# Kernel optimization log

Hardware: AMD Instinct MI355X
Metric: run time of the kernel (lower is better)

## Reference

```python
import jax, jax.numpy as jnp
import numpy as np

F = 16384   # n_features
D = 768     # d_model
B = 2       # batch
S = 256     # seq len
C = 16      # connections per downstream feature
M = F * C   # total connections


def setup_inputs() -> dict:
    key = jax.random.key(0)
    k1, k2, k3, k4 = jax.random.split(key, 4)
    up_facts = jax.random.normal(k1, (B, S, F), dtype=jnp.float32)
    down_encoder = jax.random.normal(k2, (F, D), dtype=jnp.float32) * 0.02
    up_decoder = jax.random.normal(k3, (D, F), dtype=jnp.float32) * 0.02
    # connection_mask.nonzero() is row-major: i sorted, C targets per row
    i_indices = jnp.repeat(jnp.arange(F, dtype=jnp.int32), C)  # [M]
    j_indices = jax.random.randint(k4, (M,), 0, F, dtype=jnp.int32)  # [M]
    return {
        "up_facts": up_facts,
        "down_encoder": down_encoder,
        "up_decoder": up_decoder,
        "i_indices": i_indices,
        "j_indices": j_indices,
    }


def reference(up_facts, down_encoder, up_decoder, i_indices, j_indices):
    # up_facts: [B,S,F]; down_encoder: [F,D]; up_decoder: [D,F]
    b, s, f = up_facts.shape
    m = i_indices.shape[0]
    # per-connection virtual weight: values[m] = down_encoder[i[m]] . up_decoder[:, j[m]]
    values = jnp.einsum("md,dm->m", down_encoder[i_indices], up_decoder[:, j_indices])  # [M]
    # gather upstream feature activations and scale
    scaled = up_facts[:, :, j_indices] * values[None, None, :]  # [B,S,M]
    # scatter_add over last axis into downstream feature bins (i is constant across B,S)
    flat = scaled.reshape(b * s, m).T  # [M, B*S]
    contrib = jax.ops.segment_sum(flat, i_indices, num_segments=f)  # [F, B*S]
    return contrib.T.reshape(b, s, f)
```

## Files before the change

kernel.cpp:

```cpp
#include <hip/hip_runtime.h>
#include <hip/hip_bf16.h>

#define F_ 16384
#define D_ 768
#define C_ 16
#define BS_ 512
#define M_ (F_*C_)
#define NCHUNK 8
#define CDIM 96

static __device__ __forceinline__ float bf2f(unsigned short u) {
    return __uint_as_float(((unsigned int)u) << 16);
}
static __device__ __forceinline__ unsigned short f2bf(float f) {
    return __bfloat16_as_ushort(__float2bfloat16(f));
}

__global__ __launch_bounds__(256) void k_transpose_chunked(const float* __restrict__ in,
                                                           unsigned short* __restrict__ decC) {
    __shared__ float tile[64][65];
    int c4 = threadIdx.x & 15;
    int r  = threadIdx.x >> 4;
    int fbase = blockIdx.x * 64;
    int dbase = blockIdx.y * 64;
#pragma unroll
    for (int k = 0; k < 4; ++k) {
        int drow = r + k * 16;
        float4 v = *(const float4*)(in + (size_t)(dbase + drow) * F_ + fbase + c4 * 4);
        tile[drow][c4 * 4 + 0] = v.x;
        tile[drow][c4 * 4 + 1] = v.y;
        tile[drow][c4 * 4 + 2] = v.z;
        tile[drow][c4 * 4 + 3] = v.w;
    }
    __syncthreads();
    int dp = threadIdx.x & 15;
    int fr = threadIdx.x >> 4;
#pragma unroll
    for (int k = 0; k < 4; ++k) {
        int frow = fr + k * 16;
        float v0 = tile[4 * dp + 0][frow];
        float v1 = tile[4 * dp + 1][frow];
        float v2 = tile[4 * dp + 2][frow];
        float v3 = tile[4 * dp + 3][frow];
        uint2 p;
        p.x = ((unsigned int)f2bf(v1) << 16) | (unsigned int)f2bf(v0);
        p.y = ((unsigned int)f2bf(v3) << 16) | (unsigned int)f2bf(v2);
        int d  = dbase + dp * 4;
        int c  = d / CDIM;
        int dl = d - c * CDIM;
        *(uint2*)(decC + ((size_t)c * F_ + (fbase + frow)) * CDIM + dl) = p;
    }
}

__global__ __launch_bounds__(256) void k_values_chunked(const float* __restrict__ enc,
                                                        const unsigned short* __restrict__ decC,
                                                        const int* __restrict__ jidx,
                                                        float* __restrict__ partial) {
    __shared__ float encS[64 * CDIM];
    int chunk = blockIdx.x & 7;
    int mblk  = blockIdx.x >> 3;
    int m0 = mblk * 1024;
    int f0 = mblk * 64;

    {
        float4* s4 = (float4*)encS;
        const float* eb = enc + (size_t)f0 * D_ + chunk * CDIM;
#pragma unroll
        for (int k = 0; k < 6; ++k) {
            int idx = threadIdx.x + k * 256;
            int row = idx / 24;
            int col = idx - row * 24;
            s4[row * 24 + col] = *(const float4*)(eb + (size_t)row * D_ + col * 4);
        }
    }
    __syncthreads();

    int lane = threadIdx.x & 63;
    int wave = threadIdx.x >> 6;
    int sub  = lane & 7;
    int cg   = lane >> 3;
    const unsigned short* dbase_p = decC + (size_t)chunk * F_ * CDIM;
    const float4* e4 = (const float4*)encS;

    int mmA = (wave << 3) + cg;
    int jA = jidx[m0 + mmA];
    const unsigned short* drA = dbase_p + (size_t)jA * CDIM + sub * 12;
    ushort4 g0 = *(const ushort4*)(drA);
    ushort4 g1 = *(const ushort4*)(drA + 4);
    ushort4 g2 = *(const ushort4*)(drA + 8);
    int jB = jidx[m0 + ((1 * 4 + wave) << 3) + cg];

#pragma unroll 4
    for (int i = 0; i < 32; ++i) {
        ushort4 n0, n1, n2;
        if (i + 1 < 32) {
            const unsigned short* drN = dbase_p + (size_t)jB * CDIM + sub * 12;
            n0 = *(const ushort4*)(drN);
            n1 = *(const ushort4*)(drN + 4);
            n2 = *(const ushort4*)(drN + 8);
        }
        if (i + 2 < 32)
            jB = jidx[m0 + (((i + 2) * 4 + wave) << 3) + cg];

        int mm = ((i * 4 + wave) << 3) + cg;
        int fl = mm >> 4;
        const float4* ep = e4 + fl * 24 + sub * 3;
        float4 ea = ep[0], eb = ep[1], ec = ep[2];
        float acc;
        acc  = ea.x * bf2f(g0.x) + ea.y * bf2f(g0.y) + ea.z * bf2f(g0.z) + ea.w * bf2f(g0.w);
        acc += eb.x * bf2f(g1.x) + eb.y * bf2f(g1.y) + eb.z * bf2f(g1.z) + eb.w * bf2f(g1.w);
        acc += ec.x * bf2f(g2.x) + ec.y * bf2f(g2.y) + ec.z * bf2f(g2.z) + ec.w * bf2f(g2.w);
        acc += __shfl_xor(acc, 1, 64);
        acc += __shfl_xor(acc, 2, 64);
        acc += __shfl_xor(acc, 4, 64);
        if (sub == 0)
            partial[(size_t)chunk * M_ + m0 + mm] = acc;
        g0 = n0; g1 = n1; g2 = n2;
    }
}

__global__ __launch_bounds__(256) void k_pack(const float* __restrict__ partial,
                                              const int* __restrict__ jidx,
                                              unsigned int* __restrict__ packed) {
    int m = blockIdx.x * 256 + threadIdx.x;
    float s = 0.f;
#pragma unroll
    for (int c = 0; c < NCHUNK; ++c)
        s += partial[(size_t)c * M_ + m];
    packed[m] = ((unsigned int)f2bf(s) << 16) | (unsigned int)jidx[m];
}

__global__ __launch_bounds__(512) void k_out(const float* __restrict__ up,
                                             const unsigned int* __restrict__ packed,
                                             float* __restrict__ out) {
    __shared__ unsigned int rowp[F_];
    int bs0  = (blockIdx.x >> 1) << 1;
    int half = blockIdx.x & 1;
    const float4* u0 = (const float4*)(up + (size_t)bs0 * F_);
    const float4* u1 = (const float4*)(up + (size_t)(bs0 + 1) * F_);
#pragma unroll
    for (int k = 0; k < 8; ++k) {
        int idx = threadIdx.x + k * 512;
        float4 a = u0[idx];
        float4 b = u1[idx];
        uint4 p;
        p.x = ((unsigned int)f2bf(b.x) << 16) | (unsigned int)f2bf(a.x);
        p.y = ((unsigned int)f2bf(b.y) << 16) | (unsigned int)f2bf(a.y);
        p.z = ((unsigned int)f2bf(b.z) << 16) | (unsigned int)f2bf(a.z);
        p.w = ((unsigned int)f2bf(b.w) << 16) | (unsigned int)f2bf(a.w);
        ((uint4*)rowp)[idx] = p;
    }
    __syncthreads();
    int f0 = half << 13;
#pragma unroll 4
    for (int it = 0; it < 16; ++it) {
        int f = f0 + threadIdx.x + it * 512;
        const uint4* sp = (const uint4*)(packed + ((size_t)f << 4));
        float a0 = 0.f, a1 = 0.f;
#pragma unroll
        for (int q = 0; q < 4; ++q) {
            uint4 w = sp[q];
#define CONN(ww) { unsigned int p_ = rowp[(ww) & 0xffffu];                  \
                   float v_ = __uint_as_float((ww) & 0xffff0000u);          \
                   a0 += __uint_as_float(p_ << 16) * v_;                    \
                   a1 += __uint_as_float(p_ & 0xffff0000u) * v_; }
            CONN(w.x) CONN(w.y) CONN(w.z) CONN(w.w)
#undef CONN
        }
        out[(size_t)bs0 * F_ + f] = a0;
        out[(size_t)(bs0 + 1) * F_ + f] = a1;
    }
}

extern "C" void kernel_launch(void* const* d_in, const int* in_sizes, int n_in,
                              void* d_out, int out_size, void* d_ws, size_t ws_size,
                              hipStream_t stream) {
    const float* up   = (const float*)d_in[0];
    const float* enc  = (const float*)d_in[1];
    const float* dec  = (const float*)d_in[2];
    const int*   jidx = (const int*)d_in[4];
    float*       out  = (float*)d_out;

    size_t decC_bytes    = (size_t)NCHUNK * F_ * CDIM * sizeof(unsigned short);
    size_t partial_bytes = (size_t)NCHUNK * M_ * sizeof(float);
    unsigned short* decC    = (unsigned short*)d_ws;
    float*          partial = (float*)((char*)d_ws + decC_bytes);
    unsigned int*   packed  = (unsigned int*)((char*)d_ws + decC_bytes + partial_bytes);

    k_transpose_chunked<<<dim3(F_ / 64, D_ / 64), 256, 0, stream>>>(dec, decC);
    k_values_chunked<<<NCHUNK * (M_ / 1024), 256, 0, stream>>>(enc, decC, jidx, partial);
    k_pack<<<M_ / 256, 256, 0, stream>>>(partial, jidx, packed);
    k_out<<<BS_, 512, 0, stream>>>(up, packed, out);
}
```

Measured before the change: 223.2 us.

## Use bf16 encoder tile, smaller blocks, deeper prefetch, and 1024-thread output blocks

The values kernel now stores the encoder slice in shared memory as bf16, halving LDS use. It handles 512 connections per block with occupancy hint 8, prefetches gathered decoder rows two iterations ahead using wider 16-byte and 8-byte loads, and runs half as many iterations per block. The output kernel moves to 1024-thread blocks and remaps block indices so both halves of a row pair sit farther apart in launch order. Rounding the encoder to bf16 adds precision loss, and the larger blocks may change register pressure and occupancy.

Result: slower. 229.3 us (+2.7%).

```diff
diff --git a/kernel.cpp b/kernel.cpp
--- a/kernel.cpp
+++ b/kernel.cpp
@@ -8,6 +8,8 @@
 #define M_ (F_*C_)
 #define NCHUNK 8
 #define CDIM 96
+#define CPB 512
+#define FPB (CPB/C_)
 
 static __device__ __forceinline__ float bf2f(unsigned short u) {
     return __uint_as_float(((unsigned int)u) << 16);
@@ -52,70 +54,79 @@
     }
 }
 
-__global__ __launch_bounds__(256) void k_values_chunked(const float* __restrict__ enc,
-                                                        const unsigned short* __restrict__ decC,
-                                                        const int* __restrict__ jidx,
-                                                        float* __restrict__ partial) {
-    __shared__ float encS[64 * CDIM];
+#define ACC2(e, g) {                                                         \
+    acc += __uint_as_float((e) << 16)        * __uint_as_float((g) << 16);   \
+    acc += __uint_as_float((e) & 0xffff0000u) * __uint_as_float((g) & 0xffff0000u); }
+
+__global__ __launch_bounds__(256, 8) void k_values_chunked(const float* __restrict__ enc,
+                                                           const unsigned short* __restrict__ decC,
+                                                           const int* __restrict__ jidx,
+                                                           float* __restrict__ partial) {
+    __shared__ unsigned short encS[FPB * CDIM];
     int chunk = blockIdx.x & 7;
     int mblk  = blockIdx.x >> 3;
-    int m0 = mblk * 1024;
-    int f0 = mblk * 64;
+    int m0 = mblk * CPB;
+    int f0 = mblk * FPB;
 
     {
-        float4* s4 = (float4*)encS;
         const float* eb = enc + (size_t)f0 * D_ + chunk * CDIM;
 #pragma unroll
-        for (int k = 0; k < 6; ++k) {
+        for (int k = 0; k < 3; ++k) {
             int idx = threadIdx.x + k * 256;
             int row = idx / 24;
             int col = idx - row * 24;
-            s4[row * 24 + col] = *(const float4*)(eb + (size_t)row * D_ + col * 4);
+            float4 v = *(const float4*)(eb + (size_t)row * D_ + col * 4);
+            uint2 p;
+            p.x = ((unsigned int)f2bf(v.y) << 16) | (unsigned int)f2bf(v.x);
+            p.y = ((unsigned int)f2bf(v.w) << 16) | (unsigned int)f2bf(v.z);
+            *(uint2*)(encS + row * CDIM + col * 4) = p;
         }
     }
     __syncthreads();
 
     int lane = threadIdx.x & 63;
-    int wave = threadIdx.x >> 6;
+    int w    = threadIdx.x >> 6;
     int sub  = lane & 7;
     int cg   = lane >> 3;
-    const unsigned short* dbase_p = decC + (size_t)chunk * F_ * CDIM;
-    const float4* e4 = (const float4*)encS;
-
-    int mmA = (wave << 3) + cg;
-    int jA = jidx[m0 + mmA];
-    const unsigned short* drA = dbase_p + (size_t)jA * CDIM + sub * 12;
-    ushort4 g0 = *(const ushort4*)(drA);
-    ushort4 g1 = *(const ushort4*)(drA + 4);
-    ushort4 g2 = *(const ushort4*)(drA + 8);
-    int jB = jidx[m0 + ((1 * 4 + wave) << 3) + cg];
+    const unsigned short* db = decC + (size_t)chunk * F_ * CDIM;
+
+    int j0 = jidx[m0 + ((0 * 4 + w) << 3) + cg];
+    int j1 = jidx[m0 + ((1 * 4 + w) << 3) + cg];
+    int j2 = jidx[m0 + ((2 * 4 + w) << 3) + cg];
+    const char* p0 = (const char*)(db + (size_t)j0 * CDIM) + sub * 24;
+    uint4 a0 = *(const uint4*)p0;
+    uint2 b0 = *(const uint2*)(p0 + 16);
+    const char* p1 = (const char*)(db + (size_t)j1 * CDIM) + sub * 24;
+    uint4 a1 = *(const uint4*)p1;
+    uint2 b1 = *(const uint2*)(p1 + 16);
 
 #pragma unroll 4
-    for (int i = 0; i < 32; ++i) {
-        ushort4 n0, n1, n2;
-        if (i + 1 < 32) {
-            const unsigned short* drN = dbase_p + (size_t)jB * CDIM + sub * 12;
-            n0 = *(const ushort4*)(drN);
-            n1 = *(const ushort4*)(drN + 4);
-            n2 = *(const ushort4*)(drN + 8);
+    for (int i = 0; i < 16; ++i) {
+        uint4 an; uint2 bn;
+        if (i + 2 < 16) {
+            const char* pn = (const char*)(db + (size_t)j2 * CDIM) + sub * 24;
+            an = *(const uint4*)pn;
+            bn = *(const uint2*)(pn + 16);
         }
-        if (i + 2 < 32)
-            jB = jidx[m0 + (((i + 2) * 4 + wave) << 3) + cg];
-
-        int mm = ((i * 4 + wave) << 3) + cg;
-        int fl = mm >> 4;
-        const float4* ep = e4 + fl * 24 + sub * 3;
-        float4 ea = ep[0], eb = ep[1], ec = ep[2];
-        float acc;
-        acc  = ea.x * bf2f(g0.x) + ea.y * bf2f(g0.y) + ea.z * bf2f(g0.z) + ea.w * bf2f(g0.w);
-        acc += eb.x * bf2f(g1.x) + eb.y * bf2f(g1.y) + eb.z * bf2f(g1.z) + eb.w * bf2f(g1.w);
-        acc += ec.x * bf2f(g2.x) + ec.y * bf2f(g2.y) + ec.z * bf2f(g2.z) + ec.w * bf2f(g2.w);
+        if (i + 3 < 16)
+            j2 = jidx[m0 + (((i + 3) * 4 + w) << 3) + cg];
+
+        int q  = i * 4 + w;
+        int fl = q >> 1;
+        const unsigned short* ep = encS + fl * CDIM + sub * 12;
+        uint2 e0 = *(const uint2*)ep;
+        uint2 e1 = *(const uint2*)(ep + 4);
+        uint2 e2 = *(const uint2*)(ep + 8);
+        float acc = 0.f;
+        ACC2(e0.x, a0.x) ACC2(e0.y, a0.y)
+        ACC2(e1.x, a0.z) ACC2(e1.y, a0.w)
+        ACC2(e2.x, b0.x) ACC2(e2.y, b0.y)
         acc += __shfl_xor(acc, 1, 64);
         acc += __shfl_xor(acc, 2, 64);
         acc += __shfl_xor(acc, 4, 64);
         if (sub == 0)
-            partial[(size_t)chunk * M_ + m0 + mm] = acc;
-        g0 = n0; g1 = n1; g2 = n2;
+            partial[(size_t)chunk * M_ + m0 + (q << 3) + cg] = acc;
+        a0 = a1; b0 = b1; a1 = an; b1 = bn;
     }
 }
 
@@ -130,17 +141,19 @@
     packed[m] = ((unsigned int)f2bf(s) << 16) | (unsigned int)jidx[m];
 }
 
-__global__ __launch_bounds__(512) void k_out(const float* __restrict__ up,
-                                             const unsigned int* __restrict__ packed,
-                                             float* __restrict__ out) {
+__global__ __launch_bounds__(1024) void k_out(const float* __restrict__ up,
+                                              const unsigned int* __restrict__ packed,
+                                              float* __restrict__ out) {
     __shared__ unsigned int rowp[F_];
-    int bs0  = (blockIdx.x >> 1) << 1;
-    int half = blockIdx.x & 1;
+    int x    = blockIdx.x;
+    int pair = ((x >> 4) << 3) | (x & 7);
+    int half = (x >> 3) & 1;
+    int bs0  = pair << 1;
     const float4* u0 = (const float4*)(up + (size_t)bs0 * F_);
     const float4* u1 = (const float4*)(up + (size_t)(bs0 + 1) * F_);
 #pragma unroll
-    for (int k = 0; k < 8; ++k) {
-        int idx = threadIdx.x + k * 512;
+    for (int k = 0; k < 4; ++k) {
+        int idx = threadIdx.x + k * 1024;
         float4 a = u0[idx];
         float4 b = u1[idx];
         uint4 p;
@@ -152,19 +165,19 @@
     }
     __syncthreads();
     int f0 = half << 13;
-#pragma unroll 4
-    for (int it = 0; it < 16; ++it) {
-        int f = f0 + threadIdx.x + it * 512;
+#pragma unroll 2
+    for (int it = 0; it < 8; ++it) {
+        int f = f0 + threadIdx.x + it * 1024;
         const uint4* sp = (const uint4*)(packed + ((size_t)f << 4));
         float a0 = 0.f, a1 = 0.f;
 #pragma unroll
         for (int q = 0; q < 4; ++q) {
-            uint4 w = sp[q];
+            uint4 wv = sp[q];
 #define CONN(ww) { unsigned int p_ = rowp[(ww) & 0xffffu];                  \
                    float v_ = __uint_as_float((ww) & 0xffff0000u);          \
                    a0 += __uint_as_float(p_ << 16) * v_;                    \
                    a1 += __uint_as_float(p_ & 0xffff0000u) * v_; }
-            CONN(w.x) CONN(w.y) CONN(w.z) CONN(w.w)
+            CONN(wv.x) CONN(wv.y) CONN(wv.z) CONN(wv.w)
 #undef CONN
         }
         out[(size_t)bs0 * F_ + f] = a0;
@@ -188,7 +201,7 @@
     unsigned int*   packed  = (unsigned int*)((char*)d_ws + decC_bytes + partial_bytes);
 
     k_transpose_chunked<<<dim3(F_ / 64, D_ / 64), 256, 0, stream>>>(dec, decC);
-    k_values_chunked<<<NCHUNK * (M_ / 1024), 256, 0, stream>>>(enc, decC, jidx, partial);
+    k_values_chunked<<<NCHUNK * (M_ / CPB), 256, 0, stream>>>(enc, decC, jidx, partial);
     k_pack<<<M_ / 256, 256, 0, stream>>>(partial, jidx, packed);
-    k_out<<<BS_, 512, 0, stream>>>(up, packed, out);
-}
+    k_out<<<BS_, 1024, 0, stream>>>(up, packed, out);
+}
```
